# Kernel tuning notes

Hardware: AMD Instinct MI355X
Metric: run time of the kernel (lower is better)

The kernel has to match this reference:

```python
import jax, jax.numpy as jnp
import numpy as np

B, SQ, SK, H, A = 4, 512, 512, 256, 128

def setup_inputs() -> dict:
    key = jax.random.key(0)
    ks = jax.random.split(key, 8)
    s = 1.0 / np.sqrt(H)
    sa = 1.0 / np.sqrt(A)
    return {
        "Q": jax.random.normal(ks[0], (B, SQ, H), dtype=jnp.float32),
        "K": jax.random.normal(ks[1], (B, SK, H), dtype=jnp.float32),
        "V": jax.random.normal(ks[2], (B, SK, H), dtype=jnp.float32),
        "W_q": jax.random.uniform(ks[3], (H, A), jnp.float32, -s, s),
        "W_k": jax.random.uniform(ks[4], (H, A), jnp.float32, -s, s),
        "v": jax.random.uniform(ks[5], (A,), jnp.float32, -sa, sa),
        "W_o": jax.random.uniform(ks[6], (H, H), jnp.float32, -s, s),
        "b_o": jax.random.uniform(ks[7], (H,), jnp.float32, -s, s),
    }

def reference(Q, K, V, W_q, W_k, v, W_o, b_o):
    # Q: (B, Sq, H), K/V: (B, Sk, H)
    Qt = Q @ W_q                      # (B, Sq, A)
    Kt = K @ W_k                      # (B, Sk, A)
    additive = jnp.tanh(Qt[:, :, None, :] + Kt[:, None, :, :])  # (B, Sq, Sk, A)
    scores = jnp.einsum('bqka,a->bqk', additive, v)             # (B, Sq, Sk)
    weights = jax.nn.softmax(scores, axis=-1)                   # (B, Sq, Sk)
    out = jnp.einsum('bqk,bkh->bqh', weights, V)                 # (B, Sq, H)
    out = out @ W_o + b_o
    return (out, weights)
```

## Files before the change

### kernel.cpp

```cpp
#include <hip/hip_runtime.h>
#include <math.h>

#define BB 4
#define SQL 512
#define SKL 512
#define HH 256
#define AA 128

#define PRESCALE 2.8853900817779268f

__device__ inline void fma4(float4& a, float s, const float4& b) {
    a.x = fmaf(s, b.x, a.x); a.y = fmaf(s, b.y, a.y);
    a.z = fmaf(s, b.z, a.z); a.w = fmaf(s, b.w, a.w);
}

__device__ inline unsigned short f_to_bf16(float f) {
    unsigned u = __float_as_uint(f);
    return (unsigned short)((u + 0x7fffu + ((u >> 16) & 1u)) >> 16);
}
__device__ inline float4 bf16x4_to_f4(uint2 u) {
    float4 r;
    r.x = __uint_as_float(u.x << 16);
    r.y = __uint_as_float(u.x & 0xffff0000u);
    r.z = __uint_as_float(u.y << 16);
    r.w = __uint_as_float(u.y & 0xffff0000u);
    return r;
}

__global__ __launch_bounds__(256) void prep_kernel(
    const float* __restrict__ Q, const float* __restrict__ K,
    const float* __restrict__ V,
    const float* __restrict__ Wq, const float* __restrict__ Wk,
    const float* __restrict__ Wo,
    float* __restrict__ Qt, float* __restrict__ Kt,
    unsigned short* __restrict__ VW)
{
    __shared__ float rows[16 * HH];
    __shared__ float wl[64 * 128];
    int tid = threadIdx.x;
    int bid = blockIdx.x;

    const float* X; const float* W;
    int ldW, col0, r0; float scale;
    if (bid < 128)      { X=Q; W=Wq; ldW=AA; col0=0; r0=bid*16;       scale=PRESCALE; }
    else if (bid < 256) { X=K; W=Wk; ldW=AA; col0=0; r0=(bid-128)*16; scale=PRESCALE; }
    else { int b2=bid-256; X=V; W=Wo; ldW=HH; col0=(b2&1)*128; r0=(b2>>1)*16; scale=1.0f; }

    {
        const float4* Xv = (const float4*)(X + (size_t)r0 * HH);
        float4* rv = (float4*)rows;
        rv[tid]       = Xv[tid];
        rv[tid + 256] = Xv[tid + 256];
        rv[tid + 512] = Xv[tid + 512];
        rv[tid + 768] = Xv[tid + 768];
    }

    float4 wpf[8];
    {
        const float* Wb = W + col0;
        #pragma unroll
        for (int it = 0; it < 8; ++it) {
            int l = tid + it * 256;
            wpf[it] = *(const float4*)(Wb + (size_t)(l >> 5) * ldW + ((l & 31) << 2));
        }
    }

    int r  = tid >> 5;
    int c4 = tid & 31;
    float4 accA = {0.f,0.f,0.f,0.f}, accB = {0.f,0.f,0.f,0.f};

    for (int ch = 0; ch < 4; ++ch) {
        __syncthreads();
        {
            float4* wv = (float4*)wl;
            #pragma unroll
            for (int it = 0; it < 8; ++it) wv[tid + it * 256] = wpf[it];
            if (ch < 3) {
                const float* Wb = W + (size_t)((ch + 1) * 64) * ldW + col0;
                #pragma unroll
                for (int it = 0; it < 8; ++it) {
                    int l = tid + it * 256;
                    wpf[it] = *(const float4*)(Wb + (size_t)(l >> 5) * ldW + ((l & 31) << 2));
                }
            }
        }
        __syncthreads();
        const float* rrowA = rows + r * HH + ch * 64;
        const float* rrowB = rows + (r + 8) * HH + ch * 64;
        #pragma unroll 4
        for (int h4 = 0; h4 < 16; ++h4) {
            float4 ra = *(const float4*)(rrowA + h4 * 4);
            float4 rb = *(const float4*)(rrowB + h4 * 4);
            const float* wbase = wl + (h4 * 4) * 128 + (c4 << 2);
            float4 w0 = *(const float4*)(wbase);
            float4 w1 = *(const float4*)(wbase + 128);
            float4 w2 = *(const float4*)(wbase + 256);
            float4 w3 = *(const float4*)(wbase + 384);
            fma4(accA, ra.x, w0); fma4(accA, ra.y, w1);
            fma4(accA, ra.z, w2); fma4(accA, ra.w, w3);
            fma4(accB, rb.x, w0); fma4(accB, rb.y, w1);
            fma4(accB, rb.z, w2); fma4(accB, rb.w, w3);
        }
    }

    if (bid < 256) {
        float* Y = (bid < 128) ? Qt : Kt;
        accA.x *= scale; accA.y *= scale; accA.z *= scale; accA.w *= scale;
        accB.x *= scale; accB.y *= scale; accB.z *= scale; accB.w *= scale;
        *(float4*)(Y + (size_t)(r0 + r)     * AA + (c4 << 2)) = accA;
        *(float4*)(Y + (size_t)(r0 + r + 8) * AA + (c4 << 2)) = accB;
    } else {
        ushort4 sa = { f_to_bf16(accA.x), f_to_bf16(accA.y),
                       f_to_bf16(accA.z), f_to_bf16(accA.w) };
        ushort4 sb = { f_to_bf16(accB.x), f_to_bf16(accB.y),
                       f_to_bf16(accB.z), f_to_bf16(accB.w) };
        *(ushort4*)(VW + (size_t)(r0 + r)     * HH + col0 + (c4 << 2)) = sa;
        *(ushort4*)(VW + (size_t)(r0 + r + 8) * HH + col0 + (c4 << 2)) = sb;
    }
}

__global__ __launch_bounds__(256) void score_kernel(
    const float* __restrict__ Qt, const float* __restrict__ Kt,
    const float* __restrict__ v,  const unsigned short* __restrict__ VW,
    const float* __restrict__ bo,
    float* __restrict__ weights,  float* __restrict__ out)
{
    __shared__ float score[2][SKL];
    __shared__ float pout[4][2][HH];
    __shared__ float pm[2][2], ps[2][2];

    int tid = threadIdx.x;
    int b  = blockIdx.x >> 8;
    int q0 = (blockIdx.x & 255) << 1;
    int ag = tid & 7;
    int kl = tid >> 3;

    float qreg0[16], dreg[16], v2reg[16];
    {
        const float4* vp  = (const float4*)(v + ag * 16);
        const float4* qp0 = (const float4*)(Qt + (size_t)(b * SQL + q0)     * AA + ag * 16);
        const float4* qp1 = (const float4*)(Qt + (size_t)(b * SQL + q0 + 1) * AA + ag * 16);
        #pragma unroll
        for (int j4 = 0; j4 < 4; ++j4) {
            float4 vv4 = vp[j4];
            float4 a0  = qp0[j4];
            float4 a1  = qp1[j4];
            *(float4*)&qreg0[j4 * 4] = a0;
            dreg[j4*4+0] = __builtin_amdgcn_exp2f(a1.x - a0.x);
            dreg[j4*4+1] = __builtin_amdgcn_exp2f(a1.y - a0.y);
            dreg[j4*4+2] = __builtin_amdgcn_exp2f(a1.z - a0.z);
            dreg[j4*4+3] = __builtin_amdgcn_exp2f(a1.w - a0.w);
            v2reg[j4*4+0] = 2.0f * vv4.x;
            v2reg[j4*4+1] = 2.0f * vv4.y;
            v2reg[j4*4+2] = 2.0f * vv4.z;
            v2reg[j4*4+3] = 2.0f * vv4.w;
        }
    }

    float S_all;
    {
        float ls = 0.f;
        #pragma unroll
        for (int j = 0; j < 16; ++j) ls += v2reg[j];
        ls += __shfl_xor(ls, 1);
        ls += __shfl_xor(ls, 2);
        ls += __shfl_xor(ls, 4);
        S_all = 0.5f * ls;
    }

    const float4* kp = (const float4*)(Kt + (size_t)(b * SKL + kl) * AA + ag * 16);
    float4 n0 = kp[0], n1 = kp[1], n2 = kp[2], n3 = kp[3];
    for (int c = 0; c < 16; ++c) {
        float kt[16];
        *(float4*)&kt[0]  = n0;
        *(float4*)&kt[4]  = n1;
        *(float4*)&kt[8]  = n2;
        *(float4*)&kt[12] = n3;
        if (c < 15) {
            const float4* np = kp + (size_t)(c + 1) * 32 * (AA / 4);
            n0 = np[0]; n1 = np[1]; n2 = np[2]; n3 = np[3];
        }

        float p0 = 0.f, p1 = 0.f;
        #pragma unroll
        for (int j = 0; j < 16; ++j) {
            float x0 = qreg0[j] + kt[j];
            float e0 = __builtin_amdgcn_exp2f(x0);
            float e1 = e0 * dreg[j];
            float r0 = __builtin_amdgcn_rcpf(e0 + 1.0f);
            float r1 = __builtin_amdgcn_rcpf(e1 + 1.0f);
            p0 = fmaf(v2reg[j], r0, p0);
            p1 = fmaf(v2reg[j], r1, p1);
        }
        p0 += __shfl_xor(p0, 1); p1 += __shfl_xor(p1, 1);
        p0 += __shfl_xor(p0, 2); p1 += __shfl_xor(p1, 2);
        p0 += __shfl_xor(p0, 4); p1 += __shfl_xor(p1, 4);
        if (ag == 0) {
            int k = c * 32 + kl;
            score[0][k] = S_all - p0;
            score[1][k] = S_all - p1;
        }
    }
    __syncthreads();

    int wave = tid >> 6, lane = tid & 63;
    int qi = wave & 1, half = wave >> 1;
    {
        float4* srow = (float4*)&score[qi][half * 256];
        float4 sv = srow[lane];
        float m = fmaxf(fmaxf(sv.x, sv.y), fmaxf(sv.z, sv.w));
        #pragma unroll
        for (int off = 32; off; off >>= 1) m = fmaxf(m, __shfl_xor(m, off));
        if (lane == 0) pm[qi][half] = m;
        __syncthreads();
        float M = fmaxf(pm[qi][0], pm[qi][1]);
        float4 e;
        e.x = __builtin_amdgcn_exp2f((sv.x - M) * 1.44269504f);
        e.y = __builtin_amdgcn_exp2f((sv.y - M) * 1.44269504f);
        e.z = __builtin_amdgcn_exp2f((sv.z - M) * 1.44269504f);
        e.w = __builtin_amdgcn_exp2f((sv.w - M) * 1.44269504f);
        float s = (e.x + e.y) + (e.z + e.w);
        #pragma unroll
        for (int off = 32; off; off >>= 1) s += __shfl_xor(s, off);
        if (lane == 0) ps[qi][half] = s;
        __syncthreads();
        float rinv = 1.0f / (ps[qi][0] + ps[qi][1]);
        float4 w4 = { e.x * rinv, e.y * rinv, e.z * rinv, e.w * rinv };
        srow[lane] = w4;
        *(float4*)(weights + (size_t)(b * SQL + q0 + qi) * SKL + half * 256 + (lane << 2)) = w4;
    }
    __syncthreads();

    {
        const uint2* VWb = (const uint2*)(VW + (size_t)b * SKL * HH);
        float4 a0 = {0,0,0,0}, a1 = {0,0,0,0};
        int kbase = wave * 128;
        #pragma unroll 4
        for (int k = 0; k < 128; ++k) {
            int kk = kbase + k;
            uint2 u = VWb[(size_t)kk * (HH / 4) + lane];
            float4 vw4 = bf16x4_to_f4(u);
            float w0 = score[0][kk];
            float w1 = score[1][kk];
            fma4(a0, w0, vw4);
            fma4(a1, w1, vw4);
        }
        *(float4*)&pout[wave][0][lane << 2] = a0;
        *(float4*)&pout[wave][1][lane << 2] = a1;
    }
    __syncthreads();
    {
        int h = tid;
        float bias = bo[h];
        #pragma unroll
        for (int qi2 = 0; qi2 < 2; ++qi2) {
            float s = bias + pout[0][qi2][h] + pout[1][qi2][h]
                           + pout[2][qi2][h] + pout[3][qi2][h];
            out[(size_t)(b * SQL + q0 + qi2) * HH + h] = s;
        }
    }
}

extern "C" void kernel_launch(void* const* d_in, const int* in_sizes, int n_in,
                              void* d_out, int out_size, void* d_ws, size_t ws_size,
                              hipStream_t stream)
{
    const float* Q  = (const float*)d_in[0];
    const float* K  = (const float*)d_in[1];
    const float* V  = (const float*)d_in[2];
    const float* Wq = (const float*)d_in[3];
    const float* Wk = (const float*)d_in[4];
    const float* v  = (const float*)d_in[5];
    const float* Wo = (const float*)d_in[6];
    const float* bo = (const float*)d_in[7];

    float* out     = (float*)d_out;
    float* weights = out + (size_t)BB * SQL * HH;

    float* Qt = (float*)d_ws;
    float* Kt = Qt + (size_t)BB * SQL * AA;
    unsigned short* VW = (unsigned short*)(Kt + (size_t)BB * SKL * AA);

    prep_kernel <<<512, 256, 0, stream>>>(Q, K, V, Wq, Wk, Wo, Qt, Kt, VW);
    score_kernel<<<1024, 256, 0, stream>>>(Qt, Kt, v, VW, bo, weights, out);
}
```

Baseline: 138.9 us.

## Split score kernel into score and softmax/epilogue kernels, finer prep tiling

The score kernel is split in two. One kernel computes raw additive-attention scores over half of the keys per block, using a 16-lane split of the attention dimension. It writes them to the weights buffer. A second kernel reads them back, applies softmax and does the V·W_o epilogue. The prep kernel now uses 64-column tiles with double-buffered 32-row weight chunks and twice as many blocks. The aim is more parallelism and occupancy, at the cost of a third launch and an extra global round-trip of the score matrix.

```diff
diff --git a/kernel.cpp b/kernel.cpp
--- a/kernel.cpp
+++ b/kernel.cpp
@@ -35,179 +35,177 @@
     float* __restrict__ Qt, float* __restrict__ Kt,
     unsigned short* __restrict__ VW)
 {
-    __shared__ float rows[16 * HH];
-    __shared__ float wl[64 * 128];
+    __shared__ float rows[16 * 260];
+    __shared__ float wbuf[2][32 * 64];
     int tid = threadIdx.x;
     int bid = blockIdx.x;
 
     const float* X; const float* W;
-    int ldW, col0, r0; float scale;
-    if (bid < 128)      { X=Q; W=Wq; ldW=AA; col0=0; r0=bid*16;       scale=PRESCALE; }
-    else if (bid < 256) { X=K; W=Wk; ldW=AA; col0=0; r0=(bid-128)*16; scale=PRESCALE; }
-    else { int b2=bid-256; X=V; W=Wo; ldW=HH; col0=(b2&1)*128; r0=(b2>>1)*16; scale=1.0f; }
+    int ldW, col0, r0, kind;
+    if (bid < 256)      { X=Q; W=Wq; ldW=AA; kind=0; r0=(bid>>1)*16;       col0=(bid&1)*64; }
+    else if (bid < 512) { X=K; W=Wk; ldW=AA; kind=1; r0=((bid-256)>>1)*16; col0=((bid-256)&1)*64; }
+    else { int b2=bid-512; X=V; W=Wo; ldW=HH; kind=2; r0=(b2>>2)*16;       col0=(b2&3)*64; }
 
     {
         const float4* Xv = (const float4*)(X + (size_t)r0 * HH);
-        float4* rv = (float4*)rows;
-        rv[tid]       = Xv[tid];
-        rv[tid + 256] = Xv[tid + 256];
-        rv[tid + 512] = Xv[tid + 512];
-        rv[tid + 768] = Xv[tid + 768];
-    }
-
-    float4 wpf[8];
-    {
-        const float* Wb = W + col0;
-        #pragma unroll
-        for (int it = 0; it < 8; ++it) {
+        #pragma unroll
+        for (int it = 0; it < 4; ++it) {
             int l = tid + it * 256;
-            wpf[it] = *(const float4*)(Wb + (size_t)(l >> 5) * ldW + ((l & 31) << 2));
-        }
-    }
-
-    int r  = tid >> 5;
-    int c4 = tid & 31;
-    float4 accA = {0.f,0.f,0.f,0.f}, accB = {0.f,0.f,0.f,0.f};
-
-    for (int ch = 0; ch < 4; ++ch) {
+            int rr = l >> 6, cc = (l & 63) << 2;
+            *(float4*)&rows[rr * 260 + cc] = Xv[l];
+        }
+    }
+
+    float4 wpf0, wpf1;
+    {
+        int l0 = tid, l1 = tid + 256;
+        wpf0 = *(const float4*)(W + (size_t)(l0 >> 4) * ldW + col0 + ((l0 & 15) << 2));
+        wpf1 = *(const float4*)(W + (size_t)(l1 >> 4) * ldW + col0 + ((l1 & 15) << 2));
+    }
+
+    int r  = tid >> 4;
+    int c4 = tid & 15;
+    float4 acc = {0.f, 0.f, 0.f, 0.f};
+
+    for (int c = 0; c < 8; ++c) {
+        {
+            float4* wb = (float4*)&wbuf[c & 1][0];
+            wb[tid]       = wpf0;
+            wb[tid + 256] = wpf1;
+            if (c < 7) {
+                const float* Wb = W + (size_t)((c + 1) * 32) * ldW + col0;
+                int l0 = tid, l1 = tid + 256;
+                wpf0 = *(const float4*)(Wb + (size_t)(l0 >> 4) * ldW + ((l0 & 15) << 2));
+                wpf1 = *(const float4*)(Wb + (size_t)(l1 >> 4) * ldW + ((l1 & 15) << 2));
+            }
+        }
         __syncthreads();
-        {
-            float4* wv = (float4*)wl;
-            #pragma unroll
-            for (int it = 0; it < 8; ++it) wv[tid + it * 256] = wpf[it];
-            if (ch < 3) {
-                const float* Wb = W + (size_t)((ch + 1) * 64) * ldW + col0;
-                #pragma unroll
-                for (int it = 0; it < 8; ++it) {
-                    int l = tid + it * 256;
-                    wpf[it] = *(const float4*)(Wb + (size_t)(l >> 5) * ldW + ((l & 31) << 2));
-                }
-            }
-        }
-        __syncthreads();
-        const float* rrowA = rows + r * HH + ch * 64;
-        const float* rrowB = rows + (r + 8) * HH + ch * 64;
-        #pragma unroll 4
-        for (int h4 = 0; h4 < 16; ++h4) {
-            float4 ra = *(const float4*)(rrowA + h4 * 4);
-            float4 rb = *(const float4*)(rrowB + h4 * 4);
-            const float* wbase = wl + (h4 * 4) * 128 + (c4 << 2);
-            float4 w0 = *(const float4*)(wbase);
-            float4 w1 = *(const float4*)(wbase + 128);
-            float4 w2 = *(const float4*)(wbase + 256);
-            float4 w3 = *(const float4*)(wbase + 384);
-            fma4(accA, ra.x, w0); fma4(accA, ra.y, w1);
-            fma4(accA, ra.z, w2); fma4(accA, ra.w, w3);
-            fma4(accB, rb.x, w0); fma4(accB, rb.y, w1);
-            fma4(accB, rb.z, w2); fma4(accB, rb.w, w3);
-        }
-    }
-
-    if (bid < 256) {
-        float* Y = (bid < 128) ? Qt : Kt;
-        accA.x *= scale; accA.y *= scale; accA.z *= scale; accA.w *= scale;
-        accB.x *= scale; accB.y *= scale; accB.z *= scale; accB.w *= scale;
-        *(float4*)(Y + (size_t)(r0 + r)     * AA + (c4 << 2)) = accA;
-        *(float4*)(Y + (size_t)(r0 + r + 8) * AA + (c4 << 2)) = accB;
+        const float* rrow = &rows[r * 260 + c * 32];
+        const float* wb2  = &wbuf[c & 1][c4 << 2];
+        #pragma unroll
+        for (int h = 0; h < 32; ++h) {
+            float rv  = rrow[h];
+            float4 w4 = *(const float4*)(wb2 + h * 64);
+            fma4(acc, rv, w4);
+        }
+    }
+
+    if (kind < 2) {
+        float* Y = (kind == 0) ? Qt : Kt;
+        acc.x *= PRESCALE; acc.y *= PRESCALE; acc.z *= PRESCALE; acc.w *= PRESCALE;
+        *(float4*)(Y + (size_t)(r0 + r) * AA + col0 + (c4 << 2)) = acc;
     } else {
-        ushort4 sa = { f_to_bf16(accA.x), f_to_bf16(accA.y),
-                       f_to_bf16(accA.z), f_to_bf16(accA.w) };
-        ushort4 sb = { f_to_bf16(accB.x), f_to_bf16(accB.y),
-                       f_to_bf16(accB.z), f_to_bf16(accB.w) };
-        *(ushort4*)(VW + (size_t)(r0 + r)     * HH + col0 + (c4 << 2)) = sa;
-        *(ushort4*)(VW + (size_t)(r0 + r + 8) * HH + col0 + (c4 << 2)) = sb;
-    }
-}
-
-__global__ __launch_bounds__(256) void score_kernel(
+        ushort4 s = { f_to_bf16(acc.x), f_to_bf16(acc.y),
+                      f_to_bf16(acc.z), f_to_bf16(acc.w) };
+        *(ushort4*)(VW + (size_t)(r0 + r) * HH + col0 + (c4 << 2)) = s;
+    }
+}
+
+__global__ __launch_bounds__(256) void score_part(
     const float* __restrict__ Qt, const float* __restrict__ Kt,
-    const float* __restrict__ v,  const unsigned short* __restrict__ VW,
-    const float* __restrict__ bo,
-    float* __restrict__ weights,  float* __restrict__ out)
-{
-    __shared__ float score[2][SKL];
+    const float* __restrict__ v,  float* __restrict__ scores)
+{
+    __shared__ float sc[2][256];
+
+    int tid = threadIdx.x;
+    int bid = blockIdx.x;
+    int b    = bid >> 9;
+    int rem  = bid & 511;
+    int q0   = rem & ~1;
+    int half = rem & 1;
+    int ag = tid & 15;
+    int kl = tid >> 4;
+
+    float q0r[8], dr[8], v2[8];
+    {
+        const float4* vp  = (const float4*)(v + ag * 8);
+        const float4* qp0 = (const float4*)(Qt + (size_t)(b * SQL + q0)     * AA + ag * 8);
+        const float4* qp1 = (const float4*)(Qt + (size_t)(b * SQL + q0 + 1) * AA + ag * 8);
+        #pragma unroll
+        for (int j4 = 0; j4 < 2; ++j4) {
+            float4 vv4 = vp[j4];
+            float4 a0  = qp0[j4];
+            float4 a1  = qp1[j4];
+            *(float4*)&q0r[j4 * 4] = a0;
+            dr[j4*4+0] = __builtin_amdgcn_exp2f(a1.x - a0.x);
+            dr[j4*4+1] = __builtin_amdgcn_exp2f(a1.y - a0.y);
+            dr[j4*4+2] = __builtin_amdgcn_exp2f(a1.z - a0.z);
+            dr[j4*4+3] = __builtin_amdgcn_exp2f(a1.w - a0.w);
+            v2[j4*4+0] = 2.0f * vv4.x;
+            v2[j4*4+1] = 2.0f * vv4.y;
+            v2[j4*4+2] = 2.0f * vv4.z;
+            v2[j4*4+3] = 2.0f * vv4.w;
+        }
+    }
+
+    float S_all;
+    {
+        float ls = 0.f;
+        #pragma unroll
+        for (int j = 0; j < 8; ++j) ls += v2[j];
+        ls += __shfl_xor(ls, 1);
+        ls += __shfl_xor(ls, 2);
+        ls += __shfl_xor(ls, 4);
+        ls += __shfl_xor(ls, 8);
+        S_all = 0.5f * ls;
+    }
+
+    const float4* kp = (const float4*)(Kt + (size_t)(b * SKL + half * 256 + kl) * AA + ag * 8);
+    float4 n0 = kp[0], n1 = kp[1];
+    for (int c = 0; c < 16; ++c) {
+        float kt[8];
+        *(float4*)&kt[0] = n0;
+        *(float4*)&kt[4] = n1;
+        if (c < 15) {
+            const float4* np = kp + (size_t)(c + 1) * 16 * (AA / 4);
+            n0 = np[0]; n1 = np[1];
+        }
+        float p0 = 0.f, p1 = 0.f;
+        #pragma unroll
+        for (int j = 0; j < 8; ++j) {
+            float x0 = q0r[j] + kt[j];
+            float e0 = __builtin_amdgcn_exp2f(x0);
+            float e1 = e0 * dr[j];
+            float r0 = __builtin_amdgcn_rcpf(e0 + 1.0f);
+            float r1 = __builtin_amdgcn_rcpf(e1 + 1.0f);
+            p0 = fmaf(v2[j], r0, p0);
+            p1 = fmaf(v2[j], r1, p1);
+        }
+        p0 += __shfl_xor(p0, 1); p1 += __shfl_xor(p1, 1);
+        p0 += __shfl_xor(p0, 2); p1 += __shfl_xor(p1, 2);
+        p0 += __shfl_xor(p0, 4); p1 += __shfl_xor(p1, 4);
+        p0 += __shfl_xor(p0, 8); p1 += __shfl_xor(p1, 8);
+        if (ag == 0) {
+            sc[0][c * 16 + kl] = S_all - p0;
+            sc[1][c * 16 + kl] = S_all - p1;
+        }
+    }
+    __syncthreads();
+
+    if (tid < 128) {
+        int q = tid >> 6, i = tid & 63;
+        float4 val = *(float4*)&sc[q][i << 2];
+        *(float4*)(scores + (size_t)(b * SQL + q0 + q) * SKL + half * 256 + (i << 2)) = val;
+    }
+}
+
+__global__ __launch_bounds__(256) void softepi_kernel(
+    const unsigned short* __restrict__ VW, const float* __restrict__ bo,
+    float* __restrict__ weights, float* __restrict__ out)
+{
+    __shared__ float sw[2][SKL];
     __shared__ float pout[4][2][HH];
     __shared__ float pm[2][2], ps[2][2];
 
     int tid = threadIdx.x;
     int b  = blockIdx.x >> 8;
     int q0 = (blockIdx.x & 255) << 1;
-    int ag = tid & 7;
-    int kl = tid >> 3;
-
-    float qreg0[16], dreg[16], v2reg[16];
-    {
-        const float4* vp  = (const float4*)(v + ag * 16);
-        const float4* qp0 = (const float4*)(Qt + (size_t)(b * SQL + q0)     * AA + ag * 16);
-        const float4* qp1 = (const float4*)(Qt + (size_t)(b * SQL + q0 + 1) * AA + ag * 16);
-        #pragma unroll
-        for (int j4 = 0; j4 < 4; ++j4) {
-            float4 vv4 = vp[j4];
-            float4 a0  = qp0[j4];
-            float4 a1  = qp1[j4];
-            *(float4*)&qreg0[j4 * 4] = a0;
-            dreg[j4*4+0] = __builtin_amdgcn_exp2f(a1.x - a0.x);
-            dreg[j4*4+1] = __builtin_amdgcn_exp2f(a1.y - a0.y);
-            dreg[j4*4+2] = __builtin_amdgcn_exp2f(a1.z - a0.z);
-            dreg[j4*4+3] = __builtin_amdgcn_exp2f(a1.w - a0.w);
-            v2reg[j4*4+0] = 2.0f * vv4.x;
-            v2reg[j4*4+1] = 2.0f * vv4.y;
-            v2reg[j4*4+2] = 2.0f * vv4.z;
-            v2reg[j4*4+3] = 2.0f * vv4.w;
-        }
-    }
-
-    float S_all;
-    {
-        float ls = 0.f;
-        #pragma unroll
-        for (int j = 0; j < 16; ++j) ls += v2reg[j];
-        ls += __shfl_xor(ls, 1);
-        ls += __shfl_xor(ls, 2);
-        ls += __shfl_xor(ls, 4);
-        S_all = 0.5f * ls;
-    }
-
-    const float4* kp = (const float4*)(Kt + (size_t)(b * SKL + kl) * AA + ag * 16);
-    float4 n0 = kp[0], n1 = kp[1], n2 = kp[2], n3 = kp[3];
-    for (int c = 0; c < 16; ++c) {
-        float kt[16];
-        *(float4*)&kt[0]  = n0;
-        *(float4*)&kt[4]  = n1;
-        *(float4*)&kt[8]  = n2;
-        *(float4*)&kt[12] = n3;
-        if (c < 15) {
-            const float4* np = kp + (size_t)(c + 1) * 32 * (AA / 4);
-            n0 = np[0]; n1 = np[1]; n2 = np[2]; n3 = np[3];
-        }
-
-        float p0 = 0.f, p1 = 0.f;
-        #pragma unroll
-        for (int j = 0; j < 16; ++j) {
-            float x0 = qreg0[j] + kt[j];
-            float e0 = __builtin_amdgcn_exp2f(x0);
-            float e1 = e0 * dreg[j];
-            float r0 = __builtin_amdgcn_rcpf(e0 + 1.0f);
-            float r1 = __builtin_amdgcn_rcpf(e1 + 1.0f);
-            p0 = fmaf(v2reg[j], r0, p0);
-            p1 = fmaf(v2reg[j], r1, p1);
-        }
-        p0 += __shfl_xor(p0, 1); p1 += __shfl_xor(p1, 1);
-        p0 += __shfl_xor(p0, 2); p1 += __shfl_xor(p1, 2);
-        p0 += __shfl_xor(p0, 4); p1 += __shfl_xor(p1, 4);
-        if (ag == 0) {
-            int k = c * 32 + kl;
-            score[0][k] = S_all - p0;
-            score[1][k] = S_all - p1;
-        }
-    }
-    __syncthreads();
-
     int wave = tid >> 6, lane = tid & 63;
     int qi = wave & 1, half = wave >> 1;
-    {
-        float4* srow = (float4*)&score[qi][half * 256];
-        float4 sv = srow[lane];
+
+    {
+        float* wrow = weights + (size_t)(b * SQL + q0 + qi) * SKL + half * 256;
+        float4 sv = *(float4*)(wrow + (lane << 2));
         float m = fmaxf(fmaxf(sv.x, sv.y), fmaxf(sv.z, sv.w));
         #pragma unroll
         for (int off = 32; off; off >>= 1) m = fmaxf(m, __shfl_xor(m, off));
@@ -226,8 +224,8 @@
         __syncthreads();
         float rinv = 1.0f / (ps[qi][0] + ps[qi][1]);
         float4 w4 = { e.x * rinv, e.y * rinv, e.z * rinv, e.w * rinv };
-        srow[lane] = w4;
-        *(float4*)(weights + (size_t)(b * SQL + q0 + qi) * SKL + half * 256 + (lane << 2)) = w4;
+        *(float4*)&sw[qi][half * 256 + (lane << 2)] = w4;
+        *(float4*)(wrow + (lane << 2)) = w4;
     }
     __syncthreads();
 
@@ -240,8 +238,8 @@
             int kk = kbase + k;
             uint2 u = VWb[(size_t)kk * (HH / 4) + lane];
             float4 vw4 = bf16x4_to_f4(u);
-            float w0 = score[0][kk];
-            float w1 = score[1][kk];
+            float w0 = sw[0][kk];
+            float w1 = sw[1][kk];
             fma4(a0, w0, vw4);
             fma4(a1, w1, vw4);
         }
@@ -253,10 +251,10 @@
         int h = tid;
         float bias = bo[h];
         #pragma unroll
-        for (int qi2 = 0; qi2 < 2; ++qi2) {
-            float s = bias + pout[0][qi2][h] + pout[1][qi2][h]
-                           + pout[2][qi2][h] + pout[3][qi2][h];
-            out[(size_t)(b * SQL + q0 + qi2) * HH + h] = s;
+        for (int q2 = 0; q2 < 2; ++q2) {
+            float s = bias + pout[0][q2][h] + pout[1][q2][h]
+                           + pout[2][q2][h] + pout[3][q2][h];
+            out[(size_t)(b * SQL + q0 + q2) * HH + h] = s;
         }
     }
 }
@@ -281,6 +279,7 @@
     float* Kt = Qt + (size_t)BB * SQL * AA;
     unsigned short* VW = (unsigned short*)(Kt + (size_t)BB * SKL * AA);
 
-    prep_kernel <<<512, 256, 0, stream>>>(Q, K, V, Wq, Wk, Wo, Qt, Kt, VW);
-    score_kernel<<<1024, 256, 0, stream>>>(Qt, Kt, v, VW, bo, weights, out);
-}
+    prep_kernel <<<1024, 256, 0, stream>>>(Q, K, V, Wq, Wk, Wo, Qt, Kt, VW);
+    score_part  <<<2048, 256, 0, stream>>>(Qt, Kt, v, weights);
+    softepi_kernel<<<1024, 256, 0, stream>>>(VW, bo, weights, out);
+}
```

New measurement: 130.8 us. 5.8% less time.
